# Performance work log

Hardware: AMD Instinct MI355X
Metric: run time of the kernel (lower is better)

Reference implementation:

```python
import jax, jax.numpy as jnp
import numpy as np

N = 50000   # nodes
E = 800000  # edges (avg degree 16)
G = 256     # graphs in batch
IN = 64; H = 128; K = 8; C = 10; L = 3
TAU = 1.0


def _bn(x, g, b, eps=1e-5):
    # BatchNorm1d training-mode forward: batch stats over the row dim.
    m = x.mean(0)
    v = x.var(0)
    return (x - m) * jax.lax.rsqrt(v + eps) * g + b


def _ln(x, g, b, eps=1e-5):
    m = x.mean(-1, keepdims=True)
    v = x.var(-1, keepdims=True)
    return (x - m) * jax.lax.rsqrt(v + eps) * g + b


def setup_inputs() -> dict:
    key = jax.random.key(0)
    ks = jax.random.split(key, 16)
    p = lambda k, shape: jax.random.normal(k, shape, jnp.float32) * 0.05
    u = jax.random.uniform(ks[2], (N, K), minval=1e-10, maxval=1.0)
    return {
        "x": jax.random.normal(ks[0], (N, IN), jnp.float32),
        "edge_index": jax.random.randint(ks[1], (2, E), 0, N, dtype=jnp.int32),
        "batch": (jnp.arange(N, dtype=jnp.int32) * G) // N,  # sorted, all graphs present
        "gumbel": -jnp.log(-jnp.log(u)),  # fixed Gumbel(0,1) noise
        "inp_w": p(ks[3], (IN, H)), "inp_b": jnp.zeros(H),
        "elin_w": p(ks[4], (L, 1, H)), "elin_b": jnp.zeros((L, H)),
        "mlp1_w": p(ks[5], (L, H, H)), "mlp1_b": jnp.zeros((L, H)),
        "mlpbn_g": jnp.ones((L, H)), "mlpbn_b": jnp.zeros((L, H)),
        "mlp2_w": p(ks[6], (L, H, H)), "mlp2_b": jnp.zeros((L, H)),
        "bn_g": jnp.ones((L, H)), "bn_b": jnp.zeros((L, H)),
        "bh1_w": p(ks[7], (H, H // 2)), "bh1_b": jnp.zeros(H // 2),
        "bh2_w": p(ks[8], (H // 2, K)), "bh2_b": jnp.zeros(K),
        "bm_w": p(ks[9], (H, H)), "bm_b": jnp.zeros(H),
        "ln_g": jnp.ones(H), "ln_b": jnp.zeros(H),
        "clf1_w": p(ks[10], (2 * H, H)), "clf1_b": jnp.zeros(H),
        "clfbn_g": jnp.ones(H), "clfbn_b": jnp.zeros(H),
        "clf2_w": p(ks[11], (H, C)), "clf2_b": jnp.zeros(C),
    }


def reference(x, edge_index, batch, gumbel, inp_w, inp_b, elin_w, elin_b,
              mlp1_w, mlp1_b, mlpbn_g, mlpbn_b, mlp2_w, mlp2_b, bn_g, bn_b,
              bh1_w, bh1_b, bh2_w, bh2_b, bm_w, bm_b, ln_g, ln_b,
              clf1_w, clf1_b, clfbn_g, clfbn_b, clf2_w, clf2_b):
    src, dst = edge_index[0], edge_index[1]
    h = x @ inp_w + inp_b  # [N,H]
    for l in range(L):  # GINEConv stack (eps=0, dummy edge attr = ones[E,1])
        e_emb = elin_w[l][0] + elin_b[l]          # ones @ W + b -> single [H] vector
        msg = jax.nn.relu(h[src] + e_emb)          # gather + add, [E,H]
        aggr = jax.ops.segment_sum(msg, dst, num_segments=N)  # scatter-add
        z = h + aggr                               # (1+eps)*x + aggr, eps=0
        z = jax.nn.relu(_bn(z @ mlp1_w[l] + mlp1_b[l], mlpbn_g[l], mlpbn_b[l]))
        z = z @ mlp2_w[l] + mlp2_b[l]
        h = jax.nn.relu(_bn(z, bn_g[l], bn_b[l]))
    # blob assignment via gumbel-softmax (soft)
    logits = jax.nn.relu(h @ bh1_w + bh1_b) @ bh2_w + bh2_b  # [N,K]
    assign = jax.nn.softmax((logits + gumbel) / TAU, axis=-1)
    counts = jax.ops.segment_sum(jnp.ones((N,), h.dtype), batch, num_segments=G)
    gmean = jax.ops.segment_sum(h, batch, num_segments=G) / counts[:, None]  # [G,H]
    # per-graph weighted blob pooling, vectorized over graphs via segment_sum
    num = jax.ops.segment_sum(assign[:, :, None] * h[:, None, :], batch, num_segments=G)  # [G,K,H]
    den = jax.ops.segment_sum(assign, batch, num_segments=G)  # [G,K]
    blobs = num / (den[:, :, None] + 1e-8)
    blobs = _ln(jax.nn.relu(blobs @ bm_w + bm_b), ln_g, ln_b)
    blob_emb = blobs.max(axis=1)  # [G,H]
    z = jnp.concatenate([gmean, blob_emb], axis=-1)  # [G,2H]
    z = jax.nn.relu(_bn(z @ clf1_w + clf1_b, clfbn_g, clfbn_b))
    return z @ clf2_w + clf2_b  # [G,C]
```

## Files before the change

### kernel.cpp

```cpp
#include <hip/hip_runtime.h>
#include <hip/hip_bf16.h>


#define HH 128
typedef unsigned short u16;
typedef unsigned int u32;
typedef __attribute__((ext_vector_type(8))) short bf16x8;
typedef __attribute__((ext_vector_type(4))) float f32x4;

__device__ __forceinline__ void atomAddF(float* p, float v) { unsafeAtomicAdd(p, v); }

__device__ __forceinline__ u16 f2bf(float f) {
    u32 u = __float_as_uint(f);
    u += 0x7fffu + ((u >> 16) & 1u);
    return (u16)(u >> 16);
}
__device__ __forceinline__ float bf2f_lo(u32 u) { return __uint_as_float(u << 16); }
__device__ __forceinline__ float bf2f_hi(u32 u) { return __uint_as_float(u & 0xffff0000u); }
__device__ __forceinline__ void split2(float v, u16& hi, u16& lo) {
    u16 h_ = f2bf(v);
    float hf = __uint_as_float(((u32)h_) << 16);
    hi = h_;
    lo = f2bf(v - hf);
}
__device__ __forceinline__ u32 swz(u32 row, u32 kByte, u32 strideB) {
    return (row * strideB + kByte) ^ ((row & 7u) << 4);
}

#define WTOT (8192 + 6 * 16384)

__global__ void k_prep(const float* __restrict__ inp_w, const float* __restrict__ m1,
                       const float* __restrict__ m2, u16* __restrict__ Whi,
                       u16* __restrict__ Wlo) {
    int b = blockIdx.x;
    int t = threadIdx.x;
    if (b == 0) {
        for (int idx = t; idx < 128 * 64; idx += 256) {
            int c = idx >> 6, k = idx & 63;
            u16 hi, lo;
            split2(inp_w[k * 128 + c], hi, lo);
            Whi[idx] = hi; Wlo[idx] = lo;
        }
    } else {
        const float* W = (b <= 3) ? m1 + (size_t)(b - 1) * 16384
                                  : m2 + (size_t)(b - 4) * 16384;
        u16* dh = Whi + 8192 + (size_t)(b - 1) * 16384;
        u16* dl = Wlo + 8192 + (size_t)(b - 1) * 16384;
        for (int idx = t; idx < 16384; idx += 256) {
            int c = idx >> 7, k = idx & 127;
            u16 hi, lo;
            split2(W[k * 128 + c], hi, lo);
            dh[idx] = hi; dl[idx] = lo;
        }
    }
}

__global__ void k_split(const float* __restrict__ x, u16* __restrict__ xhi,
                        u16* __restrict__ xlo, int total4) {
    int i = blockIdx.x * 256 + threadIdx.x;
    if (i >= total4) return;
    float4 v = *(const float4*)(x + (size_t)i * 4);
    u16 h0, h1, h2, h3, l0, l1, l2, l3;
    split2(v.x, h0, l0); split2(v.y, h1, l1);
    split2(v.z, h2, l2); split2(v.w, h3, l3);
    uint2 ph = {(u32)h0 | ((u32)h1 << 16), (u32)h2 | ((u32)h3 << 16)};
    uint2 pl = {(u32)l0 | ((u32)l1 << 16), (u32)l2 | ((u32)l3 << 16)};
    *(uint2*)(xhi + (size_t)i * 4) = ph;
    *(uint2*)(xlo + (size_t)i * 4) = pl;
}

__global__ void k_hist(const int* __restrict__ ei, int* __restrict__ deg, int E) {
    int i4 = blockIdx.x * 256 + threadIdx.x;
    int e0 = i4 * 4;
    if (e0 + 3 < E) {
        int4 d = *(const int4*)(ei + E + e0);
        atomicAdd(&deg[d.x], 1);
        atomicAdd(&deg[d.y], 1);
        atomicAdd(&deg[d.z], 1);
        atomicAdd(&deg[d.w], 1);
    } else {
        for (int e = e0; e < E; e++) atomicAdd(&deg[ei[E + e]], 1);
    }
}

__global__ void k_bsum(const int* __restrict__ deg, int* __restrict__ bsum, int N) {
    int t = threadIdx.x;
    int i = blockIdx.x * 256 + t;
    int v = (i < N) ? deg[i] : 0;
    for (int o = 32; o; o >>= 1) v += __shfl_down(v, o);
    __shared__ int ws_[4];
    if ((t & 63) == 0) ws_[t >> 6] = v;
    __syncthreads();
    if (t == 0) bsum[blockIdx.x] = ws_[0] + ws_[1] + ws_[2] + ws_[3];
}

__global__ void k_scan1(const int* __restrict__ bsum, int* __restrict__ boff,
                        int* __restrict__ rowptrN, int nch) {
    int t = threadIdx.x;
    int v = (t < nch) ? bsum[t] : 0;
    int l = t & 63, w = t >> 6;
    int sv = v;
    for (int o = 1; o < 64; o <<= 1) { int u = __shfl_up(sv, o); if (l >= o) sv += u; }
    __shared__ int wsum[4];
    if (l == 63) wsum[w] = sv;
    __syncthreads();
    int add = 0;
    for (int j = 0; j < w; j++) add += wsum[j];
    if (t < nch) boff[t] = sv - v + add;
    if (t == nch - 1) *rowptrN = sv + add;
}

__global__ void k_scan2(const int* __restrict__ deg, const int* __restrict__ boff,
                        int* __restrict__ rowptr, int* __restrict__ cursor, int N) {
    int b = blockIdx.x, t = threadIdx.x, i = b * 256 + t;
    int v = (i < N) ? deg[i] : 0;
    int l = t & 63, w = t >> 6;
    int sv = v;
    for (int o = 1; o < 64; o <<= 1) { int u = __shfl_up(sv, o); if (l >= o) sv += u; }
    __shared__ int wsum[4];
    if (l == 63) wsum[w] = sv;
    __syncthreads();
    int add = boff[b];
    for (int j = 0; j < w; j++) add += wsum[j];
    if (i < N) { int e = sv - v + add; rowptr[i] = e; cursor[i] = e; }
}

__global__ void k_fill(const int* __restrict__ ei, int* __restrict__ cursor,
                       int* __restrict__ col, int E) {
    int i4 = blockIdx.x * 256 + threadIdx.x;
    int e0 = i4 * 4;
    if (e0 + 3 < E) {
        int4 s = *(const int4*)(ei + e0);
        int4 d = *(const int4*)(ei + E + e0);
        int p0 = atomicAdd(&cursor[d.x], 1);
        int p1 = atomicAdd(&cursor[d.y], 1);
        int p2 = atomicAdd(&cursor[d.z], 1);
        int p3 = atomicAdd(&cursor[d.w], 1);
        col[p0] = s.x;
        col[p1] = s.y;
        col[p2] = s.z;
        col[p3] = s.w;
    } else {
        for (int e = e0; e < E; e++) {
            int pos = atomicAdd(&cursor[ei[E + e]], 1);
            col[pos] = ei[e];
        }
    }
}

template <int KD, int MODE, bool STATS, bool FOUT, bool BOUT>
__global__ __launch_bounds__(512) void k_mgemm(
    const float* __restrict__ inf, const u16* __restrict__ inhi,
    const u16* __restrict__ inlo, const u16* __restrict__ Whi,
    const u16* __restrict__ Wlo, const float* __restrict__ bias,
    const float* __restrict__ statsIn, const float* __restrict__ gamma,
    const float* __restrict__ beta, float invN,
    float* __restrict__ out, u16* __restrict__ outb,
    float* __restrict__ statsOut, int Nrows, int ntiles) {
    __shared__ u16 s_Ahi[128 * KD];
    __shared__ u16 s_Alo[128 * KD];
    __shared__ u16 s_Bhi[128 * KD];
    __shared__ u16 s_Blo[128 * KD];
    __shared__ float s_red[2][8][128];
    __shared__ float s_sc[128], s_sh[128];
    const int t = threadIdx.x;
    constexpr u32 STR = KD * 2;
    constexpr int KCB = KD / 8;
    constexpr int KCF = KD / 4;
    constexpr int NAU = (128 * KCB) / 512;
    constexpr int NAF = (128 * KCF) / 512;
    constexpr int NB  = (128 * KCB) / 512;

#pragma unroll
    for (int i = 0; i < NB; i++) {
        int idx = i * 512 + t;
        int c = idx / KCB, kc = idx % KCB;
        u32 off = swz(c, kc * 16, STR);
        *(uint4*)((char*)s_Bhi + off) = *(const uint4*)(Whi + (size_t)c * KD + kc * 8);
        *(uint4*)((char*)s_Blo + off) = *(const uint4*)(Wlo + (size_t)c * KD + kc * 8);
    }
    if (MODE == 1 && t < 128) {
        float m = statsIn[t] * invN;
        float var = statsIn[128 + t] * invN - m * m;
        float s = gamma[t] * rsqrtf(var + 1e-5f);
        s_sc[t] = s;
        s_sh[t] = beta[t] - m * s;
    }
    __syncthreads();

    float4 rf[MODE == 1 ? NAF : 1];
    uint4 rh[MODE == 2 ? NAU : 1], rl[MODE == 2 ? NAU : 1];
    int tile = blockIdx.x;
    if (tile < ntiles) {
        if (MODE == 1) {
#pragma unroll
            for (int i = 0; i < NAF; i++) {
                int idx = i * 512 + t;
                int r = idx / KCF, kc = idx % KCF;
                int gr = tile * 128 + r;
                rf[i] = (gr < Nrows) ? *(const float4*)(inf + (size_t)gr * KD + kc * 4)
                                     : (float4){0.f, 0.f, 0.f, 0.f};
            }
        } else {
#pragma unroll
            for (int i = 0; i < NAU; i++) {
                int idx = i * 512 + t;
                int r = idx / KCB, kc = idx % KCB;
                int gr = tile * 128 + r;
                if (gr < Nrows) {
                    rh[i] = *(const uint4*)(inhi + (size_t)gr * KD + kc * 8);
                    rl[i] = *(const uint4*)(inlo + (size_t)gr * KD + kc * 8);
                } else {
                    rh[i] = (uint4){0, 0, 0, 0};
                    rl[i] = (uint4){0, 0, 0, 0};
                }
            }
        }
    }

    const int l = t & 63, w = t >> 6;
    const int c0 = l & 15;
    const u32 kOffB = (u32)(l >> 4) * 16u;
    const u32 rA_row = w * 16 + c0;

    for (; tile < ntiles; tile += gridDim.x) {
        if (MODE == 1) {
#pragma unroll
            for (int i = 0; i < NAF; i++) {
                int idx = i * 512 + t;
                int r = idx / KCF, kc = idx % KCF;
                float4 v = rf[i];
                int k0 = kc * 4;
                v.x = fmaxf(v.x * s_sc[k0 + 0] + s_sh[k0 + 0], 0.f);
                v.y = fmaxf(v.y * s_sc[k0 + 1] + s_sh[k0 + 1], 0.f);
                v.z = fmaxf(v.z * s_sc[k0 + 2] + s_sh[k0 + 2], 0.f);
                v.w = fmaxf(v.w * s_sc[k0 + 3] + s_sh[k0 + 3], 0.f);
                u16 h0, h1, h2, h3, l0, l1, l2, l3;
                split2(v.x, h0, l0); split2(v.y, h1, l1);
                split2(v.z, h2, l2); split2(v.w, h3, l3);
                uint2 ph = {(u32)h0 | ((u32)h1 << 16), (u32)h2 | ((u32)h3 << 16)};
                uint2 pl = {(u32)l0 | ((u32)l1 << 16), (u32)l2 | ((u32)l3 << 16)};
                u32 off = swz(r, kc * 8, STR);
                *(uint2*)((char*)s_Ahi + off) = ph;
                *(uint2*)((char*)s_Alo + off) = pl;
            }
        } else {
#pragma unroll
            for (int i = 0; i < NAU; i++) {
                int idx = i * 512 + t;
                int r = idx / KCB, kc = idx % KCB;
                u32 off = swz(r, kc * 16, STR);
                *(uint4*)((char*)s_Ahi + off) = rh[i];
                *(uint4*)((char*)s_Alo + off) = rl[i];
            }
        }
        __syncthreads();

        int nxt = tile + gridDim.x;
        if (nxt < ntiles) {
            if (MODE == 1) {
#pragma unroll
                for (int i = 0; i < NAF; i++) {
                    int idx = i * 512 + t;
                    int r = idx / KCF, kc = idx % KCF;
                    int gr = nxt * 128 + r;
                    rf[i] = (gr < Nrows) ? *(const float4*)(inf + (size_t)gr * KD + kc * 4)
                                         : (float4){0.f, 0.f, 0.f, 0.f};
                }
            } else {
#pragma unroll
                for (int i = 0; i < NAU; i++) {
                    int idx = i * 512 + t;
                    int r = idx / KCB, kc = idx % KCB;
                    int gr = nxt * 128 + r;
                    if (gr < Nrows) {
                        rh[i] = *(const uint4*)(inhi + (size_t)gr * KD + kc * 8);
                        rl[i] = *(const uint4*)(inlo + (size_t)gr * KD + kc * 8);
                    } else {
                        rh[i] = (uint4){0, 0, 0, 0};
                        rl[i] = (uint4){0, 0, 0, 0};
                    }
                }
            }
        }

        f32x4 acc[8];
#pragma unroll
        for (int n = 0; n < 8; n++) acc[n] = (f32x4){0.f, 0.f, 0.f, 0.f};
#pragma unroll
        for (int kk = 0; kk < KD / 32; kk++) {
            u32 kb = kk * 64 + kOffB;
            bf16x8 ah = *(const bf16x8*)((char*)s_Ahi + swz(rA_row, kb, STR));
            bf16x8 al = *(const bf16x8*)((char*)s_Alo + swz(rA_row, kb, STR));
#pragma unroll
            for (int n = 0; n < 8; n++) {
                u32 ob = swz(n * 16 + c0, kb, STR);
                bf16x8 bh = *(const bf16x8*)((char*)s_Bhi + ob);
                bf16x8 bl = *(const bf16x8*)((char*)s_Blo + ob);
                acc[n] = __builtin_amdgcn_mfma_f32_16x16x32_bf16(ah, bh, acc[n], 0, 0, 0);
                acc[n] = __builtin_amdgcn_mfma_f32_16x16x32_bf16(al, bh, acc[n], 0, 0, 0);
                acc[n] = __builtin_amdgcn_mfma_f32_16x16x32_bf16(ah, bl, acc[n], 0, 0, 0);
            }
        }

        const int rbase = tile * 128 + w * 16 + ((l >> 4) << 2);
#pragma unroll
        for (int n = 0; n < 8; n++) {
            const int colc = n * 16 + c0;
            const float bv = bias[colc];
            float s = 0.f, q = 0.f;
#pragma unroll
            for (int j = 0; j < 4; j++) {
                int gr = rbase + j;
                if (gr < Nrows) {
                    float v = acc[n][j] + bv;
                    if (FOUT) out[(size_t)gr * HH + colc] = v;
                    if (BOUT) outb[(size_t)gr * HH + colc] = f2bf(v);
                    s += v;
                    q += v * v;
                }
            }
            if (STATS) {
                s += __shfl_xor(s, 16); s += __shfl_xor(s, 32);
                q += __shfl_xor(q, 16); q += __shfl_xor(q, 32);
                if (l < 16) {
                    s_red[0][w][n * 16 + l] = s;
                    s_red[1][w][n * 16 + l] = q;
                }
            }
        }
        __syncthreads();
        if (STATS && t < 128) {
            float S = 0.f, Q = 0.f;
#pragma unroll
            for (int ww = 0; ww < 8; ww++) { S += s_red[0][ww][t]; Q += s_red[1][ww][t]; }
            atomAddF(&statsOut[t], S);
            atomAddF(&statsOut[HH + t], Q);
        }
    }
}

__global__ __launch_bounds__(256) void k_gather(
    const u16* __restrict__ hb,
    const int* __restrict__ rowptr, const int* __restrict__ col,
    const float* __restrict__ ew, const float* __restrict__ eb,
    u16* __restrict__ zhi, u16* __restrict__ zlo, int N) {
    __shared__ float2 s_part[2][64];
    const int wv = threadIdx.x >> 6;
    const int lane = threadIdx.x & 63;
    const int node = blockIdx.x * 2 + (wv >> 1);
    const int hf = wv & 1;
    const int c2 = lane * 2;
    float2 acc = {0.f, 0.f};
    const bool valid = node < N;
    float2 ee = {0.f, 0.f};
    if (valid) {
        ee.x = ew[c2] + eb[c2];
        ee.y = ew[c2 + 1] + eb[c2 + 1];
        const int s = rowptr[node], eend = rowptr[node + 1];
        int e = s + hf;
        for (; e + 6 < eend; e += 8) {
            int s0 = col[e], s1 = col[e + 2], s2 = col[e + 4], s3 = col[e + 6];
            u32 u0 = *(const u32*)(hb + (size_t)s0 * HH + c2);
            u32 u1 = *(const u32*)(hb + (size_t)s1 * HH + c2);
            u32 u2 = *(const u32*)(hb + (size_t)s2 * HH + c2);
            u32 u3 = *(const u32*)(hb + (size_t)s3 * HH + c2);
            acc.x += fmaxf(bf2f_lo(u0) + ee.x, 0.f) + fmaxf(bf2f_lo(u1) + ee.x, 0.f) +
                     fmaxf(bf2f_lo(u2) + ee.x, 0.f) + fmaxf(bf2f_lo(u3) + ee.x, 0.f);
            acc.y += fmaxf(bf2f_hi(u0) + ee.y, 0.f) + fmaxf(bf2f_hi(u1) + ee.y, 0.f) +
                     fmaxf(bf2f_hi(u2) + ee.y, 0.f) + fmaxf(bf2f_hi(u3) + ee.y, 0.f);
        }
        for (; e < eend; e += 2) {
            u32 u0 = *(const u32*)(hb + (size_t)col[e] * HH + c2);
            acc.x += fmaxf(bf2f_lo(u0) + ee.x, 0.f);
            acc.y += fmaxf(bf2f_hi(u0) + ee.y, 0.f);
        }
    }
    if (hf) s_part[wv >> 1][lane] = acc;
    __syncthreads();
    if (!hf && valid) {
        float2 p = s_part[wv >> 1][lane];
        u32 un = *(const u32*)(hb + (size_t)node * HH + c2);
        float zx = bf2f_lo(un) + acc.x + p.x;
        float zy = bf2f_hi(un) + acc.y + p.y;
        u16 h0, h1, l0, l1;
        split2(zx, h0, l0);
        split2(zy, h1, l1);
        *(u32*)(zhi + (size_t)node * HH + c2) = (u32)h0 | ((u32)h1 << 16);
        *(u32*)(zlo + (size_t)node * HH + c2) = (u32)l0 | ((u32)l1 << 16);
    }
}

template <bool WF>
__global__ void k_bnrelu(const float* __restrict__ t, const float* __restrict__ stats,
                         const float* __restrict__ g, const float* __restrict__ b,
                         float invN, float* __restrict__ h, u16* __restrict__ hb,
                         int total4) {
    int i = blockIdx.x * 256 + threadIdx.x;
    if (i >= total4) return;
    int c4 = (i & 31) << 2;
    float sc[4], sh[4];
#pragma unroll
    for (int j = 0; j < 4; j++) {
        float m = stats[c4 + j] * invN;
        float var = stats[128 + c4 + j] * invN - m * m;
        float s = g[c4 + j] * rsqrtf(var + 1e-5f);
        sc[j] = s;
        sh[j] = b[c4 + j] - m * s;
    }
    float4 v = *(const float4*)(t + (size_t)i * 4);
    float4 o;
    o.x = fmaxf(v.x * sc[0] + sh[0], 0.f);
    o.y = fmaxf(v.y * sc[1] + sh[1], 0.f);
    o.z = fmaxf(v.z * sc[2] + sh[2], 0.f);
    o.w = fmaxf(v.w * sc[3] + sh[3], 0.f);
    if (WF) *(float4*)(h + (size_t)i * 4) = o;
    uint2 p = {(u32)f2bf(o.x) | ((u32)f2bf(o.y) << 16),
               (u32)f2bf(o.z) | ((u32)f2bf(o.w) << 16)};
    *(uint2*)(hb + (size_t)i * 4) = p;
}

__global__ __launch_bounds__(256) void k_assign(
    const float* __restrict__ h, const float* __restrict__ gum,
    const float* __restrict__ w1, const float* __restrict__ b1,
    const float* __restrict__ w2, const float* __restrict__ b2,
    float* __restrict__ assign, int N) {
    __shared__ float s_w1[128 * 64];
    __shared__ float s_w2[64 * 8];
    __shared__ float s_h[32][128];
    __shared__ float s_hid[32][64];
    const int t = threadIdx.x;
    const int n0 = blockIdx.x * 32;
    for (int i = t; i < 128 * 64; i += 256) s_w1[i] = w1[i];
    for (int i = t; i < 512; i += 256) s_w2[i] = w2[i];
    for (int i = t; i < 32 * 32; i += 256) {
        int r = i >> 5, c4 = (i & 31) << 2;
        int gn = n0 + r;
        float4 v = {0.f, 0.f, 0.f, 0.f};
        if (gn < N) v = *(const float4*)(h + (size_t)gn * HH + c4);
        *(float4*)(&s_h[r][c4]) = v;
    }
    __syncthreads();
    for (int o = t; o < 32 * 64; o += 256) {
        int nn = o >> 6, j = o & 63;
        float acc = b1[j];
        for (int k = 0; k < 128; k++) acc = fmaf(s_h[nn][k], s_w1[k * 64 + j], acc);
        s_hid[nn][j] = fmaxf(acc, 0.f);
    }
    __syncthreads();
    int nn = t >> 3, kk = t & 7;
    int gn = n0 + nn;
    float a = b2[kk];
    for (int j = 0; j < 64; j++) a = fmaf(s_hid[nn][j], s_w2[j * 8 + kk], a);
    if (gn < N) a += gum[(size_t)gn * 8 + kk];
    float m = a;
    m = fmaxf(m, __shfl_xor(m, 1));
    m = fmaxf(m, __shfl_xor(m, 2));
    m = fmaxf(m, __shfl_xor(m, 4));
    float e = expf(a - m);
    float s = e;
    s += __shfl_xor(s, 1); s += __shfl_xor(s, 2); s += __shfl_xor(s, 4);
    if (gn < N) assign[(size_t)gn * 8 + kk] = e / s;
}

__device__ __forceinline__ int lowerb(const int* __restrict__ arr, int n, int val) {
    int lo = 0, hi = n;
    while (lo < hi) {
        int mid = (lo + hi) >> 1;
        if (arr[mid] < val) lo = mid + 1;
        else hi = mid;
    }
    return lo;
}

__global__ __launch_bounds__(1024) void k_pool(
    const float* __restrict__ h, const float* __restrict__ assign,
    const int* __restrict__ batch, float* __restrict__ gmean,
    float* __restrict__ num, float* __restrict__ den, int N) {
    __shared__ float4 s_num[4][8][32];
    __shared__ float4 s_gm[4][32];
    __shared__ float s_den[4][8];
    const int g = blockIdx.x;
    const int t = threadIdx.x;
    const int ns = t >> 8;
    const int k = (t >> 5) & 7;
    const int lane = t & 31;
    const int c4 = lane << 2;
    const int start = lowerb(batch, N, g);
    const int end = lowerb(batch, N, g + 1);
    float4 an = {0.f, 0.f, 0.f, 0.f};
    float4 gm = {0.f, 0.f, 0.f, 0.f};
    float ad = 0.f;
    for (int n = start + ns; n < end; n += 4) {
        float a = assign[(size_t)n * 8 + k];
        const float4 hv = *(const float4*)(h + (size_t)n * HH + c4);
        an.x = fmaf(a, hv.x, an.x);
        an.y = fmaf(a, hv.y, an.y);
        an.z = fmaf(a, hv.z, an.z);
        an.w = fmaf(a, hv.w, an.w);
        if (k == 0) { gm.x += hv.x; gm.y += hv.y; gm.z += hv.z; gm.w += hv.w; }
        ad += a;
    }
    s_num[ns][k][lane] = an;
    if (k == 0) s_gm[ns][lane] = gm;
    if (lane == 0) s_den[ns][k] = ad;
    __syncthreads();
    if (t < 256) {
        float4 a0 = s_num[0][k][lane], a1 = s_num[1][k][lane];
        float4 a2 = s_num[2][k][lane], a3 = s_num[3][k][lane];
        float4 o = {a0.x + a1.x + a2.x + a3.x, a0.y + a1.y + a2.y + a3.y,
                    a0.z + a1.z + a2.z + a3.z, a0.w + a1.w + a2.w + a3.w};
        *(float4*)(num + ((size_t)g * 8 + k) * HH + c4) = o;
        if (t < 32) {
            float4 g0 = s_gm[0][lane], g1 = s_gm[1][lane];
            float4 g2 = s_gm[2][lane], g3 = s_gm[3][lane];
            int cnt = end - start;
            float inv = 1.f / (float)(cnt > 0 ? cnt : 1);
            float4 om = {(g0.x + g1.x + g2.x + g3.x) * inv,
                         (g0.y + g1.y + g2.y + g3.y) * inv,
                         (g0.z + g1.z + g2.z + g3.z) * inv,
                         (g0.w + g1.w + g2.w + g3.w) * inv};
            *(float4*)(gmean + (size_t)g * HH + c4) = om;
        }
        if (t < 8) den[(size_t)g * 8 + t] =
            s_den[0][t] + s_den[1][t] + s_den[2][t] + s_den[3][t];
    }
}

__global__ void k_blob(const float* __restrict__ num, const float* __restrict__ den,
                       const float* __restrict__ w, const float* __restrict__ b,
                       const float* __restrict__ lg, const float* __restrict__ lb,
                       float* __restrict__ blobs) {
    const int gk = blockIdx.x;
    const int c = threadIdx.x;
    __shared__ float srow[128];
    __shared__ float red[4];
    float d = den[gk] + 1e-8f;
    srow[c] = num[(size_t)gk * HH + c] / d;
    __syncthreads();
    float acc = b[c];
    for (int j = 0; j < 128; j++) acc = fmaf(srow[j], w[j * HH + c], acc);
    float y = fmaxf(acc, 0.f);
    float s = y, q = y * y;
    for (int off = 32; off > 0; off >>= 1) {
        s += __shfl_down(s, off);
        q += __shfl_down(q, off);
    }
    if ((c & 63) == 0) { red[(c >> 6) * 2] = s; red[(c >> 6) * 2 + 1] = q; }
    __syncthreads();
    float S = red[0] + red[2], Q = red[1] + red[3];
    float m = S * (1.f / 128.f);
    float var = Q * (1.f / 128.f) - m * m;
    blobs[(size_t)gk * HH + c] = (y - m) * rsqrtf(var + 1e-5f) * lg[c] + lb[c];
}

__global__ void k_clf1(const float* __restrict__ gmean, const float* __restrict__ blobs,
                       const float* __restrict__ w, const float* __restrict__ bias,
                       float* __restrict__ t4, float* __restrict__ stats) {
    int g = blockIdx.x;
    int c = threadIdx.x;
    __shared__ float s[256];
    float m = blobs[((size_t)g * 8) * HH + c];
#pragma unroll
    for (int k = 1; k < 8; k++) m = fmaxf(m, blobs[((size_t)g * 8 + k) * HH + c]);
    s[c] = gmean[(size_t)g * HH + c];
    s[128 + c] = m;
    __syncthreads();
    float acc = bias[c];
    for (int j = 0; j < 256; j++) acc = fmaf(s[j], w[j * HH + c], acc);
    t4[(size_t)g * HH + c] = acc;
    atomAddF(&stats[c], acc);
    atomAddF(&stats[HH + c], acc * acc);
}

__global__ void k_clf2(const float* __restrict__ t4, const float* __restrict__ stats,
                       const float* __restrict__ g_, const float* __restrict__ b_,
                       float invG, const float* __restrict__ w,
                       const float* __restrict__ bias, float* __restrict__ out) {
    int g = blockIdx.x;
    int t = threadIdx.x;
    __shared__ float s[128];
    float m = stats[t] * invG;
    float var = stats[128 + t] * invG - m * m;
    float sc = g_[t] * rsqrtf(var + 1e-5f);
    float sh = b_[t] - m * sc;
    s[t] = fmaxf(t4[(size_t)g * HH + t] * sc + sh, 0.f);
    __syncthreads();
    if (t < 10) {
        float acc = bias[t];
        for (int j = 0; j < 128; j++) acc = fmaf(s[j], w[j * 10 + t], acc);
        out[(size_t)g * 10 + t] = acc;
    }
}

extern "C" void kernel_launch(void* const* d_in, const int* in_sizes, int n_in,
                              void* d_out, int out_size, void* d_ws, size_t ws_size,
                              hipStream_t stream) {
    const float* x      = (const float*)d_in[0];
    const int*   ei     = (const int*)d_in[1];
    const int*   batch  = (const int*)d_in[2];
    const float* gumbel = (const float*)d_in[3];
    const float* inp_w  = (const float*)d_in[4];
    const float* inp_b  = (const float*)d_in[5];
    const float* elin_w = (const float*)d_in[6];
    const float* elin_b = (const float*)d_in[7];
    const float* mlp1_w = (const float*)d_in[8];
    const float* mlp1_b = (const float*)d_in[9];
    const float* mlpbn_g = (const float*)d_in[10];
    const float* mlpbn_b = (const float*)d_in[11];
    const float* mlp2_w = (const float*)d_in[12];
    const float* mlp2_b = (const float*)d_in[13];
    const float* bn_g   = (const float*)d_in[14];
    const float* bn_b   = (const float*)d_in[15];
    const float* bh1_w  = (const float*)d_in[16];
    const float* bh1_b  = (const float*)d_in[17];
    const float* bh2_w  = (const float*)d_in[18];
    const float* bh2_b  = (const float*)d_in[19];
    const float* bm_w   = (const float*)d_in[20];
    const float* bm_b   = (const float*)d_in[21];
    const float* ln_g   = (const float*)d_in[22];
    const float* ln_b   = (const float*)d_in[23];
    const float* clf1_w = (const float*)d_in[24];
    const float* clf1_b = (const float*)d_in[25];
    const float* clfbn_g = (const float*)d_in[26];
    const float* clfbn_b = (const float*)d_in[27];
    const float* clf2_w = (const float*)d_in[28];
    const float* clf2_b = (const float*)d_in[29];
    float* out = (float*)d_out;

    const int N = in_sizes[0] / 64;
    const int E = in_sizes[1] / 2;
    const int G = out_size / 10;

    float* ws = (float*)d_ws;
    float* h      = ws;
    float* zbuf   = h + (size_t)N * HH;
    float* t1     = zbuf + (size_t)N * HH;
    float* assign = t1 + (size_t)N * HH;
    float* gmean  = assign + (size_t)N * 8;
    float* num    = gmean + (size_t)G * HH;
    float* den    = num + (size_t)G * 8 * HH;
    float* blobs  = den + (size_t)G * 8;
    float* t4     = blobs + (size_t)G * 8 * HH;
    float* statsA = t4 + (size_t)G * HH;
    u16* Whi = (u16*)(statsA + 7 * 256);
    u16* Wlo = Whi + WTOT;
    int* rowptr = (int*)(Wlo + WTOT);
    int* cursor = rowptr + (N + 1);
    int* colidx = cursor + N;
    int* bsum   = colidx + E;
    int* boff   = bsum + 256;
    u16* hb  = (u16*)t1;
    u16* xhi = (u16*)zbuf;
    u16* xlo = xhi + (size_t)N * 64;
    u16* zhi = (u16*)zbuf;
    u16* zlo = zhi + (size_t)N * HH;
    float* t2 = zbuf;

    const dim3 B256(256), B128(128), B512(512), B1024(1024);
    const int ntiles = (N + 127) / 128;
    const int gg = ntiles < 256 ? ntiles : 256;
    const int nch = (N + 255) / 256;
    const int e4 = (E + 4 * 256 - 1) / (4 * 256);
    const float invN = 1.f / (float)N;
    const float invG = 1.f / (float)G;

    k_prep<<<7, B256, 0, stream>>>(inp_w, mlp1_w, mlp2_w, Whi, Wlo);
    hipMemsetAsync(cursor, 0, (size_t)N * sizeof(int), stream);
    hipMemsetAsync(statsA, 0, 7 * 256 * sizeof(float), stream);
    k_hist<<<e4, B256, 0, stream>>>(ei, cursor, E);
    k_bsum<<<nch, B256, 0, stream>>>(cursor, bsum, N);
    k_scan1<<<1, B256, 0, stream>>>(bsum, boff, rowptr + N, nch);
    k_scan2<<<nch, B256, 0, stream>>>(cursor, boff, rowptr, cursor, N);
    k_fill<<<e4, B256, 0, stream>>>(ei, cursor, colidx, E);
    k_split<<<(N * 16 + 255) / 256, B256, 0, stream>>>(x, xhi, xlo, N * 16);

    k_mgemm<64, 2, false, false, true><<<gg, B512, 0, stream>>>(
        nullptr, xhi, xlo, Whi, Wlo, inp_b, nullptr, nullptr, nullptr, 0.f,
        nullptr, hb, nullptr, N, ntiles);

    for (int l = 0; l < 3; l++) {
        float* sa = statsA + (size_t)(2 * l) * 256;
        float* sb = statsA + (size_t)(2 * l + 1) * 256;
        k_gather<<<(N + 1) / 2, B256, 0, stream>>>(hb, rowptr, colidx,
                                                   elin_w + l * HH, elin_b + l * HH,
                                                   zhi, zlo, N);
        k_mgemm<128, 2, true, true, false><<<gg, B512, 0, stream>>>(
            nullptr, zhi, zlo, Whi + 8192 + (size_t)l * 16384,
            Wlo + 8192 + (size_t)l * 16384, mlp1_b + l * HH,
            nullptr, nullptr, nullptr, 0.f, t1, nullptr, sa, N, ntiles);
        k_mgemm<128, 1, true, true, false><<<gg, B512, 0, stream>>>(
            t1, nullptr, nullptr, Whi + 8192 + (size_t)(3 + l) * 16384,
            Wlo + 8192 + (size_t)(3 + l) * 16384, mlp2_b + l * HH,
            sa, mlpbn_g + l * HH, mlpbn_b + l * HH, invN, t2, nullptr, sb, N, ntiles);
        if (l < 2)
            k_bnrelu<false><<<(N * 32 + 255) / 256, B256, 0, stream>>>(
                t2, sb, bn_g + l * HH, bn_b + l * HH, invN, nullptr, hb, N * 32);
        else
            k_bnrelu<true><<<(N * 32 + 255) / 256, B256, 0, stream>>>(
                t2, sb, bn_g + l * HH, bn_b + l * HH, invN, h, hb, N * 32);
    }

    k_assign<<<(N + 31) / 32, B256, 0, stream>>>(h, gumbel, bh1_w, bh1_b, bh2_w, bh2_b, assign, N);
    k_pool<<<G, B1024, 0, stream>>>(h, assign, batch, gmean, num, den, N);
    k_blob<<<G * 8, B128, 0, stream>>>(num, den, bm_w, bm_b, ln_g, ln_b, blobs);
    float* sc_ = statsA + 6 * 256;
    k_clf1<<<G, B128, 0, stream>>>(gmean, blobs, clf1_w, clf1_b, t4, sc_);
    k_clf2<<<G, B128, 0, stream>>>(t4, sc_, clfbn_g, clfbn_b, invG, clf2_w, clf2_b, out);
}
```

Measured before the change: 524.6 us.

## Fuse per-layer MLP GEMMs and BatchNorms into one cooperative kernel with grid sync

The two MLP GEMMs, both BatchNorm+ReLU steps and the final bf16 conversion of each GIN layer now run in a single cooperative kernel. Each block keeps its two row tiles' accumulators in registers and uses grid-wide syncs to wait for the global BN statistics. This removes the fp32 intermediate round trips through global memory (t1, t2) and two launches per layer. The cost is that up to 256 blocks must be co-resident, each holding 2x8 accumulator sets in registers, plus two grid barriers per layer. The input GEMM becomes a separate, simpler kernel without the register prefetch of the next tile.

After: 684.0 us. +30.4%, slower.

```diff
diff --git a/kernel.cpp b/kernel.cpp
--- a/kernel.cpp
+++ b/kernel.cpp
@@ -1,5 +1,8 @@
 #include <hip/hip_runtime.h>
 #include <hip/hip_bf16.h>
+#include <hip/hip_cooperative_groups.h>
+
+namespace cg = cooperative_groups;
 
 
 #define HH 128
@@ -148,179 +151,170 @@
     }
 }
 
-template <int KD, int MODE, bool STATS, bool FOUT, bool BOUT>
-__global__ __launch_bounds__(512) void k_mgemm(
-    const float* __restrict__ inf, const u16* __restrict__ inhi,
-    const u16* __restrict__ inlo, const u16* __restrict__ Whi,
-    const u16* __restrict__ Wlo, const float* __restrict__ bias,
-    const float* __restrict__ statsIn, const float* __restrict__ gamma,
-    const float* __restrict__ beta, float invN,
-    float* __restrict__ out, u16* __restrict__ outb,
-    float* __restrict__ statsOut, int Nrows, int ntiles) {
-    __shared__ u16 s_Ahi[128 * KD];
-    __shared__ u16 s_Alo[128 * KD];
-    __shared__ u16 s_Bhi[128 * KD];
-    __shared__ u16 s_Blo[128 * KD];
-    __shared__ float s_red[2][8][128];
-    __shared__ float s_sc[128], s_sh[128];
+__global__ __launch_bounds__(512) void k_ingemm(
+    const u16* __restrict__ xhi, const u16* __restrict__ xlo,
+    const u16* __restrict__ Whi, const u16* __restrict__ Wlo,
+    const float* __restrict__ bias, u16* __restrict__ outb,
+    int Nrows, int ntiles) {
+    constexpr int KD = 64;
+    constexpr u32 STR = 128;
+    __shared__ u16 s_A[2][128 * KD];
+    __shared__ u16 s_B[2][128 * KD];
     const int t = threadIdx.x;
-    constexpr u32 STR = KD * 2;
     constexpr int KCB = KD / 8;
-    constexpr int KCF = KD / 4;
-    constexpr int NAU = (128 * KCB) / 512;
-    constexpr int NAF = (128 * KCF) / 512;
-    constexpr int NB  = (128 * KCB) / 512;
-
-#pragma unroll
-    for (int i = 0; i < NB; i++) {
+    constexpr int NAU = 128 * KCB / 512;
+
+#pragma unroll
+    for (int i = 0; i < NAU; i++) {
         int idx = i * 512 + t;
         int c = idx / KCB, kc = idx % KCB;
         u32 off = swz(c, kc * 16, STR);
-        *(uint4*)((char*)s_Bhi + off) = *(const uint4*)(Whi + (size_t)c * KD + kc * 8);
-        *(uint4*)((char*)s_Blo + off) = *(const uint4*)(Wlo + (size_t)c * KD + kc * 8);
-    }
-    if (MODE == 1 && t < 128) {
-        float m = statsIn[t] * invN;
-        float var = statsIn[128 + t] * invN - m * m;
-        float s = gamma[t] * rsqrtf(var + 1e-5f);
-        s_sc[t] = s;
-        s_sh[t] = beta[t] - m * s;
-    }
-    __syncthreads();
-
-    float4 rf[MODE == 1 ? NAF : 1];
-    uint4 rh[MODE == 2 ? NAU : 1], rl[MODE == 2 ? NAU : 1];
-    int tile = blockIdx.x;
-    if (tile < ntiles) {
-        if (MODE == 1) {
-#pragma unroll
-            for (int i = 0; i < NAF; i++) {
-                int idx = i * 512 + t;
-                int r = idx / KCF, kc = idx % KCF;
-                int gr = tile * 128 + r;
-                rf[i] = (gr < Nrows) ? *(const float4*)(inf + (size_t)gr * KD + kc * 4)
-                                     : (float4){0.f, 0.f, 0.f, 0.f};
-            }
-        } else {
+        *(uint4*)((char*)s_B[0] + off) = *(const uint4*)(Whi + (size_t)c * KD + kc * 8);
+        *(uint4*)((char*)s_B[1] + off) = *(const uint4*)(Wlo + (size_t)c * KD + kc * 8);
+    }
+
+    const int l = t & 63, w = t >> 6;
+    const int c0 = l & 15;
+    const u32 kOffB = (u32)(l >> 4) * 16u;
+    const u32 rA_row = w * 16 + c0;
+
+    for (int tile = blockIdx.x; tile < ntiles; tile += gridDim.x) {
+#pragma unroll
+        for (int i = 0; i < NAU; i++) {
+            int idx = i * 512 + t;
+            int r = idx / KCB, kc = idx % KCB;
+            int gr = tile * 128 + r;
+            uint4 vh = {0, 0, 0, 0}, vl = {0, 0, 0, 0};
+            if (gr < Nrows) {
+                vh = *(const uint4*)(xhi + (size_t)gr * KD + kc * 8);
+                vl = *(const uint4*)(xlo + (size_t)gr * KD + kc * 8);
+            }
+            u32 off = swz(r, kc * 16, STR);
+            *(uint4*)((char*)s_A[0] + off) = vh;
+            *(uint4*)((char*)s_A[1] + off) = vl;
+        }
+        __syncthreads();
+        f32x4 acc[8];
+#pragma unroll
+        for (int n = 0; n < 8; n++) acc[n] = (f32x4){0.f, 0.f, 0.f, 0.f};
+#pragma unroll
+        for (int kk = 0; kk < KD / 32; kk++) {
+            u32 kb = kk * 64 + kOffB;
+            bf16x8 ah = *(const bf16x8*)((char*)s_A[0] + swz(rA_row, kb, STR));
+            bf16x8 al = *(const bf16x8*)((char*)s_A[1] + swz(rA_row, kb, STR));
+#pragma unroll
+            for (int n = 0; n < 8; n++) {
+                u32 ob = swz(n * 16 + c0, kb, STR);
+                bf16x8 bh = *(const bf16x8*)((char*)s_B[0] + ob);
+                bf16x8 bl = *(const bf16x8*)((char*)s_B[1] + ob);
+                acc[n] = __builtin_amdgcn_mfma_f32_16x16x32_bf16(ah, bh, acc[n], 0, 0, 0);
+                acc[n] = __builtin_amdgcn_mfma_f32_16x16x32_bf16(al, bh, acc[n], 0, 0, 0);
+                acc[n] = __builtin_amdgcn_mfma_f32_16x16x32_bf16(ah, bl, acc[n], 0, 0, 0);
+            }
+        }
+        const int rbase = tile * 128 + w * 16 + ((l >> 4) << 2);
+#pragma unroll
+        for (int n = 0; n < 8; n++) {
+            const int colc = n * 16 + c0;
+            const float bv = bias[colc];
+#pragma unroll
+            for (int j = 0; j < 4; j++) {
+                int gr = rbase + j;
+                if (gr < Nrows) outb[(size_t)gr * HH + colc] = f2bf(acc[n][j] + bv);
+            }
+        }
+        __syncthreads();
+    }
+}
+
+__global__ __launch_bounds__(512, 1) void k_layer(
+    const u16* __restrict__ zhi, const u16* __restrict__ zlo,
+    const u16* __restrict__ W1hi, const u16* __restrict__ W1lo,
+    const float* __restrict__ b1, const float* __restrict__ g1,
+    const float* __restrict__ be1,
+    const u16* __restrict__ W2hi, const u16* __restrict__ W2lo,
+    const float* __restrict__ b2, const float* __restrict__ g2,
+    const float* __restrict__ be2,
+    float* __restrict__ sa, float* __restrict__ sb, float invN,
+    u16* __restrict__ hbOut, float* __restrict__ hOut, int writeF,
+    int Nrows, int ntiles) {
+    constexpr int KD = 128;
+    constexpr u32 STR = 256;
+    __shared__ u16 s_A[2][128 * KD];
+    __shared__ u16 s_B[2][128 * KD];
+    __shared__ float s_red[2][8][128];
+    __shared__ float s_sc[128], s_sh[128];
+    cg::grid_group grid = cg::this_grid();
+    const int t = threadIdx.x;
+    const int l = t & 63, w = t >> 6;
+    const int c0 = l & 15;
+    const u32 kOffB = (u32)(l >> 4) * 16u;
+    const u32 rA_row = w * 16 + c0;
+    const int rgrp = (l >> 4) << 2;
+    constexpr int KCB = KD / 8;
+    constexpr int NAU = 128 * KCB / 512;
+
+#pragma unroll
+    for (int i = 0; i < NAU; i++) {
+        int idx = i * 512 + t;
+        int c = idx / KCB, kc = idx % KCB;
+        u32 off = swz(c, kc * 16, STR);
+        *(uint4*)((char*)s_B[0] + off) = *(const uint4*)(W1hi + (size_t)c * KD + kc * 8);
+        *(uint4*)((char*)s_B[1] + off) = *(const uint4*)(W1lo + (size_t)c * KD + kc * 8);
+    }
+
+    f32x4 acc1[2][8];
+#pragma unroll
+    for (int k = 0; k < 2; k++)
+#pragma unroll
+        for (int n = 0; n < 8; n++) acc1[k][n] = (f32x4){0.f, 0.f, 0.f, 0.f};
+
+#pragma unroll
+    for (int k = 0; k < 2; k++) {
+        int tile = blockIdx.x + k * gridDim.x;
+        if (tile < ntiles) {
 #pragma unroll
             for (int i = 0; i < NAU; i++) {
                 int idx = i * 512 + t;
                 int r = idx / KCB, kc = idx % KCB;
                 int gr = tile * 128 + r;
+                uint4 vh = {0, 0, 0, 0}, vl = {0, 0, 0, 0};
                 if (gr < Nrows) {
-                    rh[i] = *(const uint4*)(inhi + (size_t)gr * KD + kc * 8);
-                    rl[i] = *(const uint4*)(inlo + (size_t)gr * KD + kc * 8);
-                } else {
-                    rh[i] = (uint4){0, 0, 0, 0};
-                    rl[i] = (uint4){0, 0, 0, 0};
+                    vh = *(const uint4*)(zhi + (size_t)gr * KD + kc * 8);
+                    vl = *(const uint4*)(zlo + (size_t)gr * KD + kc * 8);
                 }
-            }
-        }
-    }
-
-    const int l = t & 63, w = t >> 6;
-    const int c0 = l & 15;
-    const u32 kOffB = (u32)(l >> 4) * 16u;
-    const u32 rA_row = w * 16 + c0;
-
-    for (; tile < ntiles; tile += gridDim.x) {
-        if (MODE == 1) {
-#pragma unroll
-            for (int i = 0; i < NAF; i++) {
-                int idx = i * 512 + t;
-                int r = idx / KCF, kc = idx % KCF;
-                float4 v = rf[i];
-                int k0 = kc * 4;
-                v.x = fmaxf(v.x * s_sc[k0 + 0] + s_sh[k0 + 0], 0.f);
-                v.y = fmaxf(v.y * s_sc[k0 + 1] + s_sh[k0 + 1], 0.f);
-                v.z = fmaxf(v.z * s_sc[k0 + 2] + s_sh[k0 + 2], 0.f);
-                v.w = fmaxf(v.w * s_sc[k0 + 3] + s_sh[k0 + 3], 0.f);
-                u16 h0, h1, h2, h3, l0, l1, l2, l3;
-                split2(v.x, h0, l0); split2(v.y, h1, l1);
-                split2(v.z, h2, l2); split2(v.w, h3, l3);
-                uint2 ph = {(u32)h0 | ((u32)h1 << 16), (u32)h2 | ((u32)h3 << 16)};
-                uint2 pl = {(u32)l0 | ((u32)l1 << 16), (u32)l2 | ((u32)l3 << 16)};
-                u32 off = swz(r, kc * 8, STR);
-                *(uint2*)((char*)s_Ahi + off) = ph;
-                *(uint2*)((char*)s_Alo + off) = pl;
-            }
-        } else {
-#pragma unroll
-            for (int i = 0; i < NAU; i++) {
-                int idx = i * 512 + t;
-                int r = idx / KCB, kc = idx % KCB;
                 u32 off = swz(r, kc * 16, STR);
-                *(uint4*)((char*)s_Ahi + off) = rh[i];
-                *(uint4*)((char*)s_Alo + off) = rl[i];
-            }
-        }
-        __syncthreads();
-
-        int nxt = tile + gridDim.x;
-        if (nxt < ntiles) {
-            if (MODE == 1) {
-#pragma unroll
-                for (int i = 0; i < NAF; i++) {
-                    int idx = i * 512 + t;
-                    int r = idx / KCF, kc = idx % KCF;
-                    int gr = nxt * 128 + r;
-                    rf[i] = (gr < Nrows) ? *(const float4*)(inf + (size_t)gr * KD + kc * 4)
-                                         : (float4){0.f, 0.f, 0.f, 0.f};
+                *(uint4*)((char*)s_A[0] + off) = vh;
+                *(uint4*)((char*)s_A[1] + off) = vl;
+            }
+            __syncthreads();
+#pragma unroll
+            for (int kk = 0; kk < KD / 32; kk++) {
+                u32 kb = kk * 64 + kOffB;
+                bf16x8 ah = *(const bf16x8*)((char*)s_A[0] + swz(rA_row, kb, STR));
+                bf16x8 al = *(const bf16x8*)((char*)s_A[1] + swz(rA_row, kb, STR));
+#pragma unroll
+                for (int n = 0; n < 8; n++) {
+                    u32 ob = swz(n * 16 + c0, kb, STR);
+                    bf16x8 bh = *(const bf16x8*)((char*)s_B[0] + ob);
+                    bf16x8 bl = *(const bf16x8*)((char*)s_B[1] + ob);
+                    acc1[k][n] = __builtin_amdgcn_mfma_f32_16x16x32_bf16(ah, bh, acc1[k][n], 0, 0, 0);
+                    acc1[k][n] = __builtin_amdgcn_mfma_f32_16x16x32_bf16(al, bh, acc1[k][n], 0, 0, 0);
+                    acc1[k][n] = __builtin_amdgcn_mfma_f32_16x16x32_bf16(ah, bl, acc1[k][n], 0, 0, 0);
                 }
-            } else {
-#pragma unroll
-                for (int i = 0; i < NAU; i++) {
-                    int idx = i * 512 + t;
-                    int r = idx / KCB, kc = idx % KCB;
-                    int gr = nxt * 128 + r;
-                    if (gr < Nrows) {
-                        rh[i] = *(const uint4*)(inhi + (size_t)gr * KD + kc * 8);
-                        rl[i] = *(const uint4*)(inlo + (size_t)gr * KD + kc * 8);
-                    } else {
-                        rh[i] = (uint4){0, 0, 0, 0};
-                        rl[i] = (uint4){0, 0, 0, 0};
-                    }
+            }
+            const int rbase = tile * 128 + w * 16 + rgrp;
+#pragma unroll
+            for (int n = 0; n < 8; n++) {
+                const int colc = n * 16 + c0;
+                const float bv = b1[colc];
+                float s = 0.f, q = 0.f;
+#pragma unroll
+                for (int j = 0; j < 4; j++) {
+                    float v = acc1[k][n][j] + bv;
+                    acc1[k][n][j] = v;
+                    if (rbase + j < Nrows) { s += v; q += v * v; }
                 }
-            }
-        }
-
-        f32x4 acc[8];
-#pragma unroll
-        for (int n = 0; n < 8; n++) acc[n] = (f32x4){0.f, 0.f, 0.f, 0.f};
-#pragma unroll
-        for (int kk = 0; kk < KD / 32; kk++) {
-            u32 kb = kk * 64 + kOffB;
-            bf16x8 ah = *(const bf16x8*)((char*)s_Ahi + swz(rA_row, kb, STR));
-            bf16x8 al = *(const bf16x8*)((char*)s_Alo + swz(rA_row, kb, STR));
-#pragma unroll
-            for (int n = 0; n < 8; n++) {
-                u32 ob = swz(n * 16 + c0, kb, STR);
-                bf16x8 bh = *(const bf16x8*)((char*)s_Bhi + ob);
-                bf16x8 bl = *(const bf16x8*)((char*)s_Blo + ob);
-                acc[n] = __builtin_amdgcn_mfma_f32_16x16x32_bf16(ah, bh, acc[n], 0, 0, 0);
-                acc[n] = __builtin_amdgcn_mfma_f32_16x16x32_bf16(al, bh, acc[n], 0, 0, 0);
-                acc[n] = __builtin_amdgcn_mfma_f32_16x16x32_bf16(ah, bl, acc[n], 0, 0, 0);
-            }
-        }
-
-        const int rbase = tile * 128 + w * 16 + ((l >> 4) << 2);
-#pragma unroll
-        for (int n = 0; n < 8; n++) {
-            const int colc = n * 16 + c0;
-            const float bv = bias[colc];
-            float s = 0.f, q = 0.f;
-#pragma unroll
-            for (int j = 0; j < 4; j++) {
-                int gr = rbase + j;
-                if (gr < Nrows) {
-                    float v = acc[n][j] + bv;
-                    if (FOUT) out[(size_t)gr * HH + colc] = v;
-                    if (BOUT) outb[(size_t)gr * HH + colc] = f2bf(v);
-                    s += v;
-                    q += v * v;
-                }
-            }
-            if (STATS) {
                 s += __shfl_xor(s, 16); s += __shfl_xor(s, 32);
                 q += __shfl_xor(q, 16); q += __shfl_xor(q, 32);
                 if (l < 16) {
@@ -328,14 +322,136 @@
                     s_red[1][w][n * 16 + l] = q;
                 }
             }
-        }
-        __syncthreads();
-        if (STATS && t < 128) {
-            float S = 0.f, Q = 0.f;
-#pragma unroll
-            for (int ww = 0; ww < 8; ww++) { S += s_red[0][ww][t]; Q += s_red[1][ww][t]; }
-            atomAddF(&statsOut[t], S);
-            atomAddF(&statsOut[HH + t], Q);
+            __syncthreads();
+            if (t < 128) {
+                float S = 0.f, Q = 0.f;
+#pragma unroll
+                for (int ww = 0; ww < 8; ww++) { S += s_red[0][ww][t]; Q += s_red[1][ww][t]; }
+                atomAddF(&sa[t], S);
+                atomAddF(&sa[HH + t], Q);
+            }
+            __syncthreads();
+        }
+    }
+    grid.sync();
+
+    if (t < 128) {
+        float m = sa[t] * invN;
+        float var = sa[128 + t] * invN - m * m;
+        float s = g1[t] * rsqrtf(var + 1e-5f);
+        s_sc[t] = s;
+        s_sh[t] = be1[t] - m * s;
+    }
+#pragma unroll
+    for (int i = 0; i < NAU; i++) {
+        int idx = i * 512 + t;
+        int c = idx / KCB, kc = idx % KCB;
+        u32 off = swz(c, kc * 16, STR);
+        *(uint4*)((char*)s_B[0] + off) = *(const uint4*)(W2hi + (size_t)c * KD + kc * 8);
+        *(uint4*)((char*)s_B[1] + off) = *(const uint4*)(W2lo + (size_t)c * KD + kc * 8);
+    }
+    __syncthreads();
+
+    f32x4 acc2[2][8];
+#pragma unroll
+    for (int k = 0; k < 2; k++)
+#pragma unroll
+        for (int n = 0; n < 8; n++) acc2[k][n] = (f32x4){0.f, 0.f, 0.f, 0.f};
+
+#pragma unroll
+    for (int k = 0; k < 2; k++) {
+        int tile = blockIdx.x + k * gridDim.x;
+        if (tile < ntiles) {
+#pragma unroll
+            for (int n = 0; n < 8; n++) {
+                const int colc = n * 16 + c0;
+                const float sc = s_sc[colc], sh = s_sh[colc];
+#pragma unroll
+                for (int j = 0; j < 4; j++) {
+                    int rloc = w * 16 + rgrp + j;
+                    float v = fmaxf(acc1[k][n][j] * sc + sh, 0.f);
+                    u16 hi, lo;
+                    split2(v, hi, lo);
+                    u32 off = swz(rloc, (u32)colc * 2, STR);
+                    *(u16*)((char*)s_A[0] + off) = hi;
+                    *(u16*)((char*)s_A[1] + off) = lo;
+                }
+            }
+            __syncthreads();
+#pragma unroll
+            for (int kk = 0; kk < KD / 32; kk++) {
+                u32 kb = kk * 64 + kOffB;
+                bf16x8 ah = *(const bf16x8*)((char*)s_A[0] + swz(rA_row, kb, STR));
+                bf16x8 al = *(const bf16x8*)((char*)s_A[1] + swz(rA_row, kb, STR));
+#pragma unroll
+                for (int n = 0; n < 8; n++) {
+                    u32 ob = swz(n * 16 + c0, kb, STR);
+                    bf16x8 bh = *(const bf16x8*)((char*)s_B[0] + ob);
+                    bf16x8 bl = *(const bf16x8*)((char*)s_B[1] + ob);
+                    acc2[k][n] = __builtin_amdgcn_mfma_f32_16x16x32_bf16(ah, bh, acc2[k][n], 0, 0, 0);
+                    acc2[k][n] = __builtin_amdgcn_mfma_f32_16x16x32_bf16(al, bh, acc2[k][n], 0, 0, 0);
+                    acc2[k][n] = __builtin_amdgcn_mfma_f32_16x16x32_bf16(ah, bl, acc2[k][n], 0, 0, 0);
+                }
+            }
+            const int rbase = tile * 128 + w * 16 + rgrp;
+#pragma unroll
+            for (int n = 0; n < 8; n++) {
+                const int colc = n * 16 + c0;
+                const float bv = b2[colc];
+                float s = 0.f, q = 0.f;
+#pragma unroll
+                for (int j = 0; j < 4; j++) {
+                    float v = acc2[k][n][j] + bv;
+                    acc2[k][n][j] = v;
+                    if (rbase + j < Nrows) { s += v; q += v * v; }
+                }
+                s += __shfl_xor(s, 16); s += __shfl_xor(s, 32);
+                q += __shfl_xor(q, 16); q += __shfl_xor(q, 32);
+                if (l < 16) {
+                    s_red[0][w][n * 16 + l] = s;
+                    s_red[1][w][n * 16 + l] = q;
+                }
+            }
+            __syncthreads();
+            if (t < 128) {
+                float S = 0.f, Q = 0.f;
+#pragma unroll
+                for (int ww = 0; ww < 8; ww++) { S += s_red[0][ww][t]; Q += s_red[1][ww][t]; }
+                atomAddF(&sb[t], S);
+                atomAddF(&sb[HH + t], Q);
+            }
+            __syncthreads();
+        }
+    }
+    grid.sync();
+
+    if (t < 128) {
+        float m = sb[t] * invN;
+        float var = sb[128 + t] * invN - m * m;
+        float s = g2[t] * rsqrtf(var + 1e-5f);
+        s_sc[t] = s;
+        s_sh[t] = be2[t] - m * s;
+    }
+    __syncthreads();
+#pragma unroll
+    for (int k = 0; k < 2; k++) {
+        int tile = blockIdx.x + k * gridDim.x;
+        if (tile < ntiles) {
+            const int rbase = tile * 128 + w * 16 + rgrp;
+#pragma unroll
+            for (int n = 0; n < 8; n++) {
+                const int colc = n * 16 + c0;
+                const float sc = s_sc[colc], sh = s_sh[colc];
+#pragma unroll
+                for (int j = 0; j < 4; j++) {
+                    int gr = rbase + j;
+                    if (gr < Nrows) {
+                        float v = fmaxf(acc2[k][n][j] * sc + sh, 0.f);
+                        hbOut[(size_t)gr * HH + colc] = f2bf(v);
+                        if (writeF) hOut[(size_t)gr * HH + colc] = v;
+                    }
+                }
+            }
         }
     }
 }
@@ -389,35 +505,6 @@
         *(u32*)(zhi + (size_t)node * HH + c2) = (u32)h0 | ((u32)h1 << 16);
         *(u32*)(zlo + (size_t)node * HH + c2) = (u32)l0 | ((u32)l1 << 16);
     }
-}
-
-template <bool WF>
-__global__ void k_bnrelu(const float* __restrict__ t, const float* __restrict__ stats,
-                         const float* __restrict__ g, const float* __restrict__ b,
-                         float invN, float* __restrict__ h, u16* __restrict__ hb,
-                         int total4) {
-    int i = blockIdx.x * 256 + threadIdx.x;
-    if (i >= total4) return;
-    int c4 = (i & 31) << 2;
-    float sc[4], sh[4];
-#pragma unroll
-    for (int j = 0; j < 4; j++) {
-        float m = stats[c4 + j] * invN;
-        float var = stats[128 + c4 + j] * invN - m * m;
-        float s = g[c4 + j] * rsqrtf(var + 1e-5f);
-        sc[j] = s;
-        sh[j] = b[c4 + j] - m * s;
-    }
-    float4 v = *(const float4*)(t + (size_t)i * 4);
-    float4 o;
-    o.x = fmaxf(v.x * sc[0] + sh[0], 0.f);
-    o.y = fmaxf(v.y * sc[1] + sh[1], 0.f);
-    o.z = fmaxf(v.z * sc[2] + sh[2], 0.f);
-    o.w = fmaxf(v.w * sc[3] + sh[3], 0.f);
-    if (WF) *(float4*)(h + (size_t)i * 4) = o;
-    uint2 p = {(u32)f2bf(o.x) | ((u32)f2bf(o.y) << 16),
-               (u32)f2bf(o.z) | ((u32)f2bf(o.w) << 16)};
-    *(uint2*)(hb + (size_t)i * 4) = p;
 }
 
 __global__ __launch_bounds__(256) void k_assign(
@@ -655,7 +742,6 @@
     u16* xlo = xhi + (size_t)N * 64;
     u16* zhi = (u16*)zbuf;
     u16* zlo = zhi + (size_t)N * HH;
-    float* t2 = zbuf;
 
     const dim3 B256(256), B128(128), B512(512), B1024(1024);
     const int ntiles = (N + 127) / 128;
@@ -675,30 +761,38 @@
     k_fill<<<e4, B256, 0, stream>>>(ei, cursor, colidx, E);
     k_split<<<(N * 16 + 255) / 256, B256, 0, stream>>>(x, xhi, xlo, N * 16);
 
-    k_mgemm<64, 2, false, false, true><<<gg, B512, 0, stream>>>(
-        nullptr, xhi, xlo, Whi, Wlo, inp_b, nullptr, nullptr, nullptr, 0.f,
-        nullptr, hb, nullptr, N, ntiles);
+    k_ingemm<<<gg, B512, 0, stream>>>(xhi, xlo, Whi, Wlo, inp_b, hb, N, ntiles);
 
     for (int l = 0; l < 3; l++) {
         float* sa = statsA + (size_t)(2 * l) * 256;
-        float* sb = statsA + (size_t)(2 * l + 1) * 256;
+        float* sb = sa + 256;
         k_gather<<<(N + 1) / 2, B256, 0, stream>>>(hb, rowptr, colidx,
                                                    elin_w + l * HH, elin_b + l * HH,
                                                    zhi, zlo, N);
-        k_mgemm<128, 2, true, true, false><<<gg, B512, 0, stream>>>(
-            nullptr, zhi, zlo, Whi + 8192 + (size_t)l * 16384,
-            Wlo + 8192 + (size_t)l * 16384, mlp1_b + l * HH,
-            nullptr, nullptr, nullptr, 0.f, t1, nullptr, sa, N, ntiles);
-        k_mgemm<128, 1, true, true, false><<<gg, B512, 0, stream>>>(
-            t1, nullptr, nullptr, Whi + 8192 + (size_t)(3 + l) * 16384,
-            Wlo + 8192 + (size_t)(3 + l) * 16384, mlp2_b + l * HH,
-            sa, mlpbn_g + l * HH, mlpbn_b + l * HH, invN, t2, nullptr, sb, N, ntiles);
-        if (l < 2)
-            k_bnrelu<false><<<(N * 32 + 255) / 256, B256, 0, stream>>>(
-                t2, sb, bn_g + l * HH, bn_b + l * HH, invN, nullptr, hb, N * 32);
-        else
-            k_bnrelu<true><<<(N * 32 + 255) / 256, B256, 0, stream>>>(
-                t2, sb, bn_g + l * HH, bn_b + l * HH, invN, h, hb, N * 32);
+        const u16* W1h = Whi + 8192 + (size_t)l * 16384;
+        const u16* W1l = Wlo + 8192 + (size_t)l * 16384;
+        const u16* W2h = Whi + 8192 + (size_t)(3 + l) * 16384;
+        const u16* W2l = Wlo + 8192 + (size_t)(3 + l) * 16384;
+        const float* b1p = mlp1_b + l * HH;
+        const float* g1p = mlpbn_g + l * HH;
+        const float* be1p = mlpbn_b + l * HH;
+        const float* b2p = mlp2_b + l * HH;
+        const float* g2p = bn_g + l * HH;
+        const float* be2p = bn_b + l * HH;
+        const u16* zhc = zhi; const u16* zlc = zlo;
+        u16* hbp = hb;
+        float* hp = h;
+        int writeF = (l == 2) ? 1 : 0;
+        float invNv = invN;
+        int Nv = N, ntv = ntiles;
+        void* args[] = {(void*)&zhc, (void*)&zlc, (void*)&W1h, (void*)&W1l,
+                        (void*)&b1p, (void*)&g1p, (void*)&be1p,
+                        (void*)&W2h, (void*)&W2l, (void*)&b2p, (void*)&g2p,
+                        (void*)&be2p, (void*)&sa, (void*)&sb, (void*)&invNv,
+                        (void*)&hbp, (void*)&hp, (void*)&writeF,
+                        (void*)&Nv, (void*)&ntv};
+        hipLaunchCooperativeKernel((const void*)k_layer, dim3(gg), dim3(512),
+                                   args, 0, stream);
     }
 
     k_assign<<<(N + 31) / 32, B256, 0, stream>>>(h, gumbel, bh1_w, bh1_b, bh2_w, bh2_b, assign, N);
```
